# Performance work log

Hardware: AMD Instinct MI355X
Metric: run time of the kernel (lower is better)

The kernel has to match this reference:

```python
import jax, jax.numpy as jnp
import numpy as np

B, W, KD, NC, D, NN, NH, AD, HOPS = 512, 4, 64, 32, 256, 16, 8, 32, 4
DH = D // NH
DFF = 4 * D
P = B * W + B
ROLE_WRITER, ROLE_QUERY = 0, 1


def setup_inputs() -> dict:
    key = jax.random.key(0)
    ks = iter(jax.random.split(key, 40))
    f = lambda shape, s=0.02: jax.random.normal(next(ks), shape, dtype=jnp.float32) * s
    inp = {
        'query_keys': jax.random.normal(next(ks), (B, KD), dtype=jnp.float32),
        'writer_keys': jax.random.normal(next(ks), (B, W, KD), dtype=jnp.float32),
        'key_proj_w': f((KD, D)), 'key_proj_b': jnp.zeros((D,), jnp.float32),
        'class_embed': f((NC, D)), 'role_embed': f((3, D)), 'start_node_embed': f((NN, D)),
        'input_ln_g': jnp.ones((D,), jnp.float32), 'input_ln_b': jnp.zeros((D,), jnp.float32),
        'ln1_g': jnp.ones((NN, D), jnp.float32), 'ln1_b': jnp.zeros((NN, D), jnp.float32),
        'wqkv': f((NN, D, 3 * D)), 'bqkv': jnp.zeros((NN, 3 * D), jnp.float32),
        'wo': f((NN, D, D)), 'bo': jnp.zeros((NN, D), jnp.float32),
        'ln2_g': jnp.ones((NN, D), jnp.float32), 'ln2_b': jnp.zeros((NN, D), jnp.float32),
        'w_fc1': f((NN, D, DFF)), 'b_fc1': jnp.zeros((NN, DFF), jnp.float32),
        'w_fc2': f((NN, DFF, D)), 'b_fc2': jnp.zeros((NN, D), jnp.float32),
        'delta_w': jnp.zeros((D, D), jnp.float32), 'delta_b': jnp.zeros((D,), jnp.float32),
        'dir_w': f((D, D)), 'dir_b': jnp.zeros((D,), jnp.float32),
        'mag_w': f((D, 1)), 'mag_b': jnp.full((1,), 2.5, jnp.float32),
        'out_w': f((D, NC)), 'out_b': jnp.zeros((NC,), jnp.float32),
        'address_table': jax.random.normal(next(ks), (NN, AD), dtype=jnp.float32),
        'query_start_nodes': jax.random.randint(next(ks), (B,), 0, NN),
        'writer_labels': jax.random.randint(next(ks), (B, W), 0, NC),
        'writer_start_nodes': jax.random.randint(next(ks), (B, W), 0, NN),
    }
    return inp


def _ln(x):
    m = jnp.mean(x, -1, keepdims=True)
    v = jnp.var(x, -1, keepdims=True)
    return (x - m) * jax.lax.rsqrt(v + 1e-5)


def _forward(query_keys, writer_keys, key_proj_w, key_proj_b, class_embed, role_embed,
             start_node_embed, input_ln_g, input_ln_b, ln1_g, ln1_b, wqkv, bqkv, wo, bo,
             ln2_g, ln2_b, w_fc1, b_fc1, w_fc2, b_fc2, delta_w, delta_b, dir_w, dir_b,
             mag_w, mag_b, out_w, out_b, address_table,
             query_start_nodes, writer_labels, writer_start_nodes):
    # ---- encode writers (encode_writers) ----
    fk = writer_keys.reshape(-1, KD)          # [B*W, KD]
    fl = writer_labels.reshape(-1)            # [B*W]
    fs = writer_start_nodes.reshape(-1)       # [B*W]
    learned_w = fk @ key_proj_w + key_proj_b + class_embed[fl] + start_node_embed[fs] + role_embed[ROLE_WRITER]
    sw = jnp.zeros_like(learned_w).at[:, :KD].set(fk)
    sw = sw.at[:, KD:KD + NC].set(jax.nn.one_hot(fl, NC, dtype=learned_w.dtype))
    enc_w = _ln(learned_w) * input_ln_g + input_ln_b + sw
    # ---- encode queries (encode_queries) ----
    learned_q = query_keys @ key_proj_w + key_proj_b + start_node_embed[query_start_nodes] + role_embed[ROLE_QUERY]
    sq = jnp.zeros_like(learned_q).at[:, :KD].set(query_keys)
    enc_q = _ln(learned_q) * input_ln_g + input_ln_b + sq

    h = jnp.concatenate([enc_w, enc_q], axis=0)          # [P, D]
    node = jnp.concatenate([fs, query_start_nodes], 0)   # [P] current compute node per packet

    inv_sqrt_dh = 1.0 / np.sqrt(DH).astype(np.float32)
    for _ in range(HOPS):
        oh = jax.nn.one_hot(node, NN, dtype=h.dtype)      # [P, NN] dispatch weights

        def pnl(x, Wn, bn):
            # per-node linear: gather-compute-scatter via MoE-style dense dispatch
            xe = jnp.einsum('pn,pd->npd', oh, x)          # [NN, P, din]
            ye = jnp.einsum('npd,ndf->npf', xe, Wn)       # [NN, P, dout]
            return jnp.einsum('npf,pn->pf', ye, oh) + oh @ bn

        # ComputeNodeCell: pre-LN attention among packets at the same node
        x = _ln(h) * (oh @ ln1_g) + oh @ ln1_b
        qkv = pnl(x, wqkv, bqkv)                          # [P, 3D]
        q, k, v = jnp.split(qkv, 3, axis=-1)
        q = q.reshape(P, NH, DH); k = k.reshape(P, NH, DH); v = v.reshape(P, NH, DH)
        scores = jnp.einsum('phd,qhd->hpq', q, k) * inv_sqrt_dh   # [NH, P, P]
        same = node[:, None] == node[None, :]
        scores = jnp.where(same[None], scores, -1e9)
        attn = jax.nn.softmax(scores, axis=-1)
        ao = jnp.einsum('hpq,qhd->phd', attn, v).reshape(P, D)
        h = h + pnl(ao, wo, bo)
        # MLP block
        x2 = _ln(h) * (oh @ ln2_g) + oh @ ln2_b
        h = h + pnl(jax.nn.gelu(pnl(x2, w_fc1, b_fc1)), w_fc2, b_fc2)
        # routing heads: pick next node from address table, apply gated delta
        direction = h @ dir_w + dir_b
        node = jnp.argmax(direction[:, :AD] @ address_table.T, axis=-1)
        h = h + (h @ delta_w + delta_b) * jax.nn.sigmoid(h @ mag_w + mag_b)

    return h @ out_w + out_b                              # [P, NC] per-packet logits


def reference(query_keys, writer_keys, key_proj_w, key_proj_b, class_embed, role_embed,
              start_node_embed, input_ln_g, input_ln_b, ln1_g, ln1_b, wqkv, bqkv, wo, bo,
              ln2_g, ln2_b, w_fc1, b_fc1, w_fc2, b_fc2, delta_w, delta_b, dir_w, dir_b,
              mag_w, mag_b, out_w, out_b, address_table,
              query_start_nodes, writer_labels, writer_start_nodes):
    return _forward(query_keys, writer_keys, key_proj_w, key_proj_b, class_embed, role_embed,
                    start_node_embed, input_ln_g, input_ln_b, ln1_g, ln1_b, wqkv, bqkv, wo, bo,
                    ln2_g, ln2_b, w_fc1, b_fc1, w_fc2, b_fc2, delta_w, delta_b, dir_w, dir_b,
                    mag_w, mag_b, out_w, out_b, address_table,
                    query_start_nodes, writer_labels, writer_start_nodes)
```

## Files before the change

kernel.cpp:

```cpp
#include <hip/hip_runtime.h>
#include <math.h>

#define B_    512
#define W_    4
#define KD_   64
#define NC_   32
#define D_    256
#define NN_   16
#define NH_   8
#define AD_   32
#define HOPS_ 4
#define DH_   32
#define DFF_  1024
#define P_    2560
#define BW_   2048
#define MAXT_  56
#define MAXT2_ 176
#define PS_   (P_ + 16)

#define INV_SQRT_DH 0.17677669529663687f

typedef __attribute__((ext_vector_type(8))) short short8v;
typedef __attribute__((ext_vector_type(4))) float f32x4;

__device__ __forceinline__ unsigned short bf16_rne(float f) {
  unsigned u = __float_as_uint(f);
  unsigned r = (u + 0x7fffu + ((u >> 16) & 1u)) >> 16;
  return (unsigned short)r;
}
__device__ __forceinline__ void split2(float v, unsigned short& h, unsigned short& l) {
  unsigned short hb = bf16_rne(v);
  float hf = __uint_as_float(((unsigned)hb) << 16);
  h = hb;
  l = bf16_rne(v - hf);
}

__device__ __forceinline__ float block_sum256(float v, float* red) {
#pragma unroll
  for (int off = 32; off > 0; off >>= 1) v += __shfl_xor(v, off, 64);
  int wid = threadIdx.x >> 6;
  if ((threadIdx.x & 63) == 0) red[wid] = v;
  __syncthreads();
  float s = red[0] + red[1] + red[2] + red[3];
  __syncthreads();
  return s;
}

__device__ __forceinline__ float gelu_tanh(float v) {
  float u = 0.7978845608028654f * (v + 0.044715f * v * v * v);
  return 0.5f * v * (1.0f + tanhf(u));
}

__global__ __launch_bounds__(256) void padzero_kernel(unsigned short* __restrict__ xh,
                                                      unsigned short* __restrict__ xl,
                                                      unsigned short* __restrict__ ffh,
                                                      unsigned short* __restrict__ ffl) {
  int t = threadIdx.x;
  for (int i = t; i < 16 * D_; i += 256) {
    xh[(size_t)P_ * D_ + i] = 0;
    xl[(size_t)P_ * D_ + i] = 0;
  }
  for (int i = t; i < 16 * DFF_; i += 256) {
    ffh[(size_t)P_ * DFF_ + i] = 0;
    ffl[(size_t)P_ * DFF_ + i] = 0;
  }
}

__global__ __launch_bounds__(256) void encode_kernel(
    const float* __restrict__ query_keys, const float* __restrict__ writer_keys,
    const float* __restrict__ kpw, const float* __restrict__ kpb,
    const float* __restrict__ ce, const float* __restrict__ re,
    const float* __restrict__ sne, const float* __restrict__ ilg,
    const float* __restrict__ ilb, const int* __restrict__ qsn,
    const int* __restrict__ wl, const int* __restrict__ wsn,
    float* __restrict__ h, int* __restrict__ node) {
  int p = blockIdx.x, t = threadIdx.x;
  __shared__ float fk[KD_];
  __shared__ float red[4];
  const float* key;
  int lab = -1, sn, role;
  if (p < BW_) { key = writer_keys + (size_t)p * KD_; lab = wl[p]; sn = wsn[p]; role = 0; }
  else { int b = p - BW_; key = query_keys + (size_t)b * KD_; sn = qsn[b]; role = 1; }
  if (t < KD_) fk[t] = key[t];
  __syncthreads();

  float acc = kpb[t] + sne[sn * D_ + t] + re[role * D_ + t];
  if (lab >= 0) acc += ce[lab * D_ + t];
#pragma unroll 8
  for (int i = 0; i < KD_; i++) acc += fk[i] * kpw[i * D_ + t];

  float mean = block_sum256(acc, red) * (1.0f / D_);
  float d = acc - mean;
  float var = block_sum256(d * d, red) * (1.0f / D_);
  float xn = d * (1.0f / sqrtf(var + 1e-5f));

  float sw = 0.0f;
  if (t < KD_) sw = fk[t];
  else if (lab >= 0 && t < KD_ + NC_) sw = (t - KD_ == lab) ? 1.0f : 0.0f;

  h[(size_t)p * D_ + t] = xn * ilg[t] + ilb[t] + sw;
  if (t == 0) node[p] = sn;
}

__global__ __launch_bounds__(256) void sort_kernel(const int* __restrict__ node,
                                                   int* __restrict__ order,
                                                   int* __restrict__ invord,
                                                   int* __restrict__ offs,
                                                   int* __restrict__ cnts,
                                                   int* __restrict__ tnode64,
                                                   int* __restrict__ tstart64,
                                                   int* __restrict__ tend64,
                                                   int* __restrict__ ntiles64,
                                                   int* __restrict__ tnode16,
                                                   int* __restrict__ tstart16,
                                                   int* __restrict__ tend16,
                                                   int* __restrict__ ntiles16) {
  __shared__ int c[NN_], o[NN_], cur[NN_];
  int t = threadIdx.x;
  if (t < NN_) c[t] = 0;
  __syncthreads();
  for (int p = t; p < P_; p += 256) atomicAdd(&c[node[p]], 1);
  __syncthreads();
  if (t == 0) {
    int s = 0;
    for (int n = 0; n < NN_; n++) { o[n] = s; cur[n] = s; s += c[n]; }
    int i64 = 0, i16 = 0;
    for (int n = 0; n < NN_; n++) {
      int e = o[n] + c[n];
      for (int m0 = o[n]; m0 < e; m0 += 64) {
        tnode64[i64] = n; tstart64[i64] = m0; tend64[i64] = e; i64++;
      }
      for (int m0 = o[n]; m0 < e; m0 += 16) {
        tnode16[i16] = n; tstart16[i16] = m0; tend16[i16] = e; i16++;
      }
    }
    ntiles64[0] = i64;
    ntiles16[0] = i16;
  }
  __syncthreads();
  if (t < NN_) { cnts[t] = c[t]; offs[t] = o[t]; }
  for (int p = t; p < P_; p += 256) {
    int r = atomicAdd(&cur[node[p]], 1);
    order[r] = p;
    invord[p] = r;
  }
}

__global__ __launch_bounds__(256) void ln_affine(const float* __restrict__ h,
                                                 const float* __restrict__ g,
                                                 const float* __restrict__ b,
                                                 const int* __restrict__ node,
                                                 const int* __restrict__ order,
                                                 unsigned short* __restrict__ xh,
                                                 unsigned short* __restrict__ xl) {
  int sp = blockIdx.x * 4 + (threadIdx.x >> 6);
  int lane = threadIdx.x & 63;
  int p = order[sp];
  int n = node[p];
  float4 v = *(const float4*)&h[(size_t)p * D_ + lane * 4];
  float s = v.x + v.y + v.z + v.w;
#pragma unroll
  for (int off = 32; off > 0; off >>= 1) s += __shfl_xor(s, off, 64);
  float mean = s * (1.0f / D_);
  float4 d = make_float4(v.x - mean, v.y - mean, v.z - mean, v.w - mean);
  float vr = d.x * d.x + d.y * d.y + d.z * d.z + d.w * d.w;
#pragma unroll
  for (int off = 32; off > 0; off >>= 1) vr += __shfl_xor(vr, off, 64);
  float inv = 1.0f / sqrtf(vr * (1.0f / D_) + 1e-5f);
  float4 gg = *(const float4*)&g[n * D_ + lane * 4];
  float4 bb = *(const float4*)&b[n * D_ + lane * 4];
  float o[4];
  o[0] = d.x * inv * gg.x + bb.x;
  o[1] = d.y * inv * gg.y + bb.y;
  o[2] = d.z * inv * gg.z + bb.z;
  o[3] = d.w * inv * gg.w + bb.w;
  ushort4 oh, ol;
  split2(o[0], oh.x, ol.x);
  split2(o[1], oh.y, ol.y);
  split2(o[2], oh.z, ol.z);
  split2(o[3], oh.w, ol.w);
  *(ushort4*)&xh[(size_t)sp * D_ + lane * 4] = oh;
  *(ushort4*)&xl[(size_t)sp * D_ + lane * 4] = ol;
}

template <int K, int C>
__global__ __launch_bounds__(256) void wprep(const float* __restrict__ W,
                                             unsigned short* __restrict__ th,
                                             unsigned short* __restrict__ tl) {
  __shared__ float ld[32][33];
  int n = blockIdx.z;
  int k0 = blockIdx.x * 32, c0 = blockIdx.y * 32;
  int tx = threadIdx.x & 31, ty = threadIdx.x >> 5;
  const float* Wn = W + (size_t)n * K * C;
#pragma unroll
  for (int i = 0; i < 32; i += 8)
    ld[i + ty][tx] = Wn[(size_t)(k0 + i + ty) * C + c0 + tx];
  __syncthreads();
#pragma unroll
  for (int i = 0; i < 32; i += 8) {
    float v = ld[tx][i + ty];
    unsigned short hh, ll;
    split2(v, hh, ll);
    size_t off = ((size_t)n * C + c0 + i + ty) * K + k0 + tx;
    th[off] = hh;
    tl[off] = ll;
  }
}

template <int DIN, int DOUT, int ACT, int RESID, int SPLITOUT>
__global__ __launch_bounds__(256) void gmfma(
    const unsigned short* __restrict__ xh, const unsigned short* __restrict__ xl,
    const unsigned short* __restrict__ wth, const unsigned short* __restrict__ wtl,
    const float* __restrict__ bias, float* __restrict__ outf,
    unsigned short* __restrict__ outh, unsigned short* __restrict__ outl,
    const int* __restrict__ order, const int* __restrict__ tnode,
    const int* __restrict__ tstart, const int* __restrict__ tend,
    const int* __restrict__ ntiles) {
  constexpr int NCH = DIN / 64;
  __shared__ unsigned short ws[2][2][64][64];

  int gx = gridDim.x;
  int bid = blockIdx.x;
  int ti = (bid & 7) * (gx >> 3) + (bid >> 3);
  if (ti >= ntiles[0]) return;
  int n = tnode[ti];
  int s0 = tstart[ti];
  int rows = tend[ti] - s0;
  if (rows <= 0) return;
  if (rows > 16) rows = 16;

  int tid = threadIdx.x;
  int wv = tid >> 6;
  int lane = tid & 63;
  int r16 = lane & 15;
  int kg = lane >> 4;
  int jb = blockIdx.y * 64;

  const unsigned short* wsrc[4];
  int sj[4], c0j[4];
#pragma unroll
  for (int jj = 0; jj < 4; jj++) {
    int j = wv * 4 + jj;
    int s = j >> 3;
    int c0 = (j & 7) * 8;
    int c = c0 + (lane >> 3);
    int e = (lane & 7) ^ (c & 7);
    wsrc[jj] = ((e & 4) ? wtl : wth) +
               ((size_t)(n * DOUT + jb + c)) * DIN + s * 32 + (e & 3) * 8;
    sj[jj] = s;
    c0j[jj] = c0;
  }
  auto stage = [&](int buf, int kbase) {
#pragma unroll
    for (int jj = 0; jj < 4; jj++) {
      __builtin_amdgcn_global_load_lds(
          (const __attribute__((address_space(1))) unsigned int*)(wsrc[jj] + kbase),
          (__attribute__((address_space(3))) unsigned int*)&ws[buf][sj[jj]][c0j[jj]][0],
          16, 0, 0);
    }
  };

  const unsigned short* pah = xh + (size_t)(s0 + r16) * DIN + kg * 8;
  const unsigned short* pal = xl + (size_t)(s0 + r16) * DIN + kg * 8;

  short8v ah[2], al[2], nh[2], nl[2];
  auto afetch = [&](int kbase, short8v (&h_)[2], short8v (&l_)[2]) {
#pragma unroll
    for (int s = 0; s < 2; s++) {
      h_[s] = *(const short8v*)(pah + kbase + s * 32);
      l_[s] = *(const short8v*)(pal + kbase + s * 32);
    }
  };

  f32x4 acc0 = {0.f, 0.f, 0.f, 0.f};
  f32x4 acc1 = acc0, acc2 = acc0;
  int lcol = wv * 16 + r16;
  int ghi_ = (kg ^ (r16 & 7)) * 8;
  int glo_ = ((4 + kg) ^ (r16 & 7)) * 8;

  stage(0, 0);
  afetch(0, ah, al);
  __syncthreads();

  for (int ch = 0; ch < NCH; ch++) {
    int cur = ch & 1;
    if (ch + 1 < NCH) {
      stage(cur ^ 1, (ch + 1) * 64);
      afetch((ch + 1) * 64, nh, nl);
    }
#pragma unroll
    for (int s = 0; s < 2; s++) {
      short8v bh = *(const short8v*)&ws[cur][s][lcol][ghi_];
      short8v bl = *(const short8v*)&ws[cur][s][lcol][glo_];
      acc0 = __builtin_amdgcn_mfma_f32_16x16x32_bf16(ah[s], bh, acc0, 0, 0, 0);
      acc1 = __builtin_amdgcn_mfma_f32_16x16x32_bf16(ah[s], bl, acc1, 0, 0, 0);
      acc2 = __builtin_amdgcn_mfma_f32_16x16x32_bf16(al[s], bh, acc2, 0, 0, 0);
    }
    __syncthreads();
    if (ch + 1 < NCH) {
#pragma unroll
      for (int s = 0; s < 2; s++) { ah[s] = nh[s]; al[s] = nl[s]; }
    }
  }

  int jcol = jb + wv * 16;
  float bv = bias[(size_t)n * DOUT + jcol + r16];
#pragma unroll
  for (int rg = 0; rg < 4; rg++) {
    int r = kg * 4 + rg;
    if (r >= rows) continue;
    float v = acc0[rg] + acc1[rg] + acc2[rg] + bv;
    if (ACT) v = gelu_tanh(v);
    if (SPLITOUT) {
      size_t off = (size_t)(s0 + r) * DOUT + jcol + r16;
      unsigned short hh, ll;
      split2(v, hh, ll);
      outh[off] = hh;
      outl[off] = ll;
    } else if (RESID) {
      int pp = order[s0 + r];
      float* op = outf + (size_t)pp * DOUT + jcol + r16;
      *op += v;
    } else {
      outf[(size_t)(s0 + r) * DOUT + jcol + r16] = v;
    }
  }
}

template <int DIN, int DOUT, int JT, int ACT, int RESID, int PER_NODE, int KSPLIT, int XMODE>
__global__ __launch_bounds__(256) void glin(const float* __restrict__ x,
                                            const float* __restrict__ W,
                                            const float* __restrict__ bias,
                                            float* __restrict__ out,
                                            float* __restrict__ pbuf,
                                            const float* __restrict__ xaux,
                                            const int* __restrict__ order,
                                            const int* __restrict__ invord,
                                            const int* __restrict__ tnode,
                                            const int* __restrict__ tstart,
                                            const int* __restrict__ tend,
                                            const int* __restrict__ ntiles) {
  constexpr int KC = 32, STX = 68;
  constexpr int CPT = JT / 16;
  constexpr int HALF = 64;
  constexpr int KLEN = DIN / KSPLIT;
  constexpr int NCH = KLEN / KC;
  constexpr int LPR = JT / 4;
  constexpr int RPI = 64 / LPR;

  int ti = blockIdx.x;
  int n, s0, s1;
  if (PER_NODE) {
    if (ti >= ntiles[0]) return;
    n = tnode[ti]; s0 = tstart[ti]; s1 = tend[ti];
  } else {
    n = 0; s0 = ti * 64; s1 = P_;
  }
  int jbase = blockIdx.y * JT;
  int kz = (KSPLIT > 1) ? blockIdx.z : 0;
  int k0 = kz * KLEN;
  int rows = s1 - s0; if (rows > 64) rows = 64;

  __shared__ float xs[2][KC][STX];
  __shared__ float ws[2][KC][JT];

  int tid = threadIdx.x;
  const float* Wn = W + (size_t)n * DIN * DOUT + jbase;

  int xrow = tid >> 2, xq = tid & 3;
  bool xvalid = xrow < rows;
  const float* xptr = x + (size_t)(s0 + (xvalid ? xrow : 0)) * DIN + k0 + xq * 4;
  const float* aptr = nullptr;
  if (XMODE == 1) {
    int pr = xvalid ? invord[s0 + xrow] : 0;
    aptr = xaux + (size_t)pr * DIN + k0 + xq * 4;
  }

  float4 xr0, xr1;
  auto xfetch = [&](int kc) {
    if (xvalid) {
      xr0 = *(const float4*)(xptr + kc);
      xr1 = *(const float4*)(xptr + kc + 16);
      if (XMODE == 1) {
        float4 p0 = *(const float4*)(aptr + kc);
        float4 p1 = *(const float4*)(aptr + kc + 16);
        xr0.x += p0.x; xr0.y += p0.y; xr0.z += p0.z; xr0.w += p0.w;
        xr1.x += p1.x; xr1.y += p1.y; xr1.z += p1.z; xr1.w += p1.w;
      }
    } else {
      xr0 = make_float4(0.f, 0.f, 0.f, 0.f);
      xr1 = make_float4(0.f, 0.f, 0.f, 0.f);
    }
  };
  auto xstage = [&](int buf) {
    xs[buf][xq * 4 + 0][xrow] = xr0.x;
    xs[buf][xq * 4 + 1][xrow] = xr0.y;
    xs[buf][xq * 4 + 2][xrow] = xr0.z;
    xs[buf][xq * 4 + 3][xrow] = xr0.w;
    xs[buf][xq * 4 + 16][xrow] = xr1.x;
    xs[buf][xq * 4 + 17][xrow] = xr1.y;
    xs[buf][xq * 4 + 18][xrow] = xr1.z;
    xs[buf][xq * 4 + 19][xrow] = xr1.w;
  };
  int wvw = tid >> 6, lane = tid & 63;
  int wlr = lane / LPR;
  int wlc = (lane % LPR) * 4;
  auto wfetch = [&](int buf, int kc) {
#pragma unroll
    for (int i = 0; i < 8 / RPI; i++) {
      int kr = wvw * 8 + i * RPI;
      const float* g = &Wn[(size_t)(k0 + kc + kr + wlr) * DOUT + wlc];
      __builtin_amdgcn_global_load_lds(
          (const __attribute__((address_space(1))) unsigned int*)g,
          (__attribute__((address_space(3))) unsigned int*)&ws[buf][kr][0],
          16, 0, 0);
    }
  };

  wfetch(0, 0);
  xfetch(0);
  xstage(0);
  __syncthreads();

  int r4 = (tid >> 4) * 4;
  int jc4 = (tid & 15) * 4;
  float acc[4][CPT];
#pragma unroll
  for (int r = 0; r < 4; r++)
#pragma unroll
    for (int cc = 0; cc < CPT; cc++) acc[r][cc] = 0.f;

  for (int c = 0; c < NCH; c++) {
    int cur = c & 1;
    if (c + 1 < NCH) {
      wfetch(cur ^ 1, (c + 1) * KC);
      xfetch((c + 1) * KC);
    }
#pragma unroll 8
    for (int k = 0; k < KC; k++) {
      float4 a = *(const float4*)&xs[cur][k][r4];
      float av[4] = {a.x, a.y, a.z, a.w};
      float bv[CPT];
      float4 b0 = *(const float4*)&ws[cur][k][jc4];
      bv[0] = b0.x; bv[1] = b0.y; bv[2] = b0.z; bv[3] = b0.w;
      if (CPT == 8) {
        float4 b1 = *(const float4*)&ws[cur][k][jc4 + HALF];
        bv[4] = b1.x; bv[5] = b1.y; bv[6] = b1.z; bv[7] = b1.w;
      }
#pragma unroll
      for (int r = 0; r < 4; r++)
#pragma unroll
        for (int cc = 0; cc < CPT; cc++) acc[r][cc] += av[r] * bv[cc];
    }
    if (c + 1 < NCH) xstage(cur ^ 1);
    __syncthreads();
  }

  bool main_part = (KSPLIT == 1) || (kz == 0);
  float bbv[CPT];
#pragma unroll
  for (int cc = 0; cc < 4; cc++) bbv[cc] = bias[n * DOUT + jbase + jc4 + cc];
  if (CPT == 8) {
#pragma unroll
    for (int cc = 0; cc < 4; cc++) bbv[4 + cc] = bias[n * DOUT + jbase + jc4 + HALF + cc];
  }

#pragma unroll
  for (int r = 0; r < 4; r++) {
    int lr = r4 + r;
    if (lr >= rows) continue;
    float v[CPT];
    if (main_part) {
#pragma unroll
      for (int cc = 0; cc < CPT; cc++) {
        v[cc] = acc[r][cc] + bbv[cc];
        if (ACT == 1) v[cc] = gelu_tanh(v[cc]);
      }
      if (RESID) {
        int pp = PER_NODE ? order[s0 + lr] : (s0 + lr);
        float* op = &out[(size_t)pp * DOUT + jbase + jc4];
        {
          float4 old = *(const float4*)op;
          *(float4*)op = make_float4(v[0] + old.x, v[1] + old.y, v[2] + old.z, v[3] + old.w);
        }
        if (CPT == 8) {
          float4 old = *(const float4*)(op + HALF);
          *(float4*)(op + HALF) =
              make_float4(v[4] + old.x, v[5] + old.y, v[6] + old.z, v[7] + old.w);
        }
      } else {
        float* op = &out[(size_t)(s0 + lr) * DOUT + jbase + jc4];
        *(float4*)op = make_float4(v[0], v[1], v[2], v[3]);
        if (CPT == 8)
          *(float4*)(op + HALF) = make_float4(v[4], v[5], v[6], v[7]);
      }
    } else {
      float* op = &pbuf[(size_t)(s0 + lr) * DOUT + jbase + jc4];
      *(float4*)op = make_float4(acc[r][0], acc[r][1], acc[r][2], acc[r][3]);
      if (CPT == 8)
        *(float4*)(op + HALF) = make_float4(acc[r][4], acc[r][5], acc[r][6], acc[r][7]);
    }
  }
}

#define ATS 36
__global__ __launch_bounds__(256) void attn_kernel(const float* __restrict__ qkv,
                                                   const int* __restrict__ node,
                                                   const int* __restrict__ order,
                                                   const int* __restrict__ offs,
                                                   const int* __restrict__ cnts,
                                                   float* __restrict__ ao) {
  __shared__ float qs[32 * ATS];
  __shared__ float kts[32 * ATS];
  __shared__ float vs[32 * ATS];
  __shared__ float ps[32 * ATS];
  __shared__ int glo[32], ghi[32];

  int t = threadIdx.x;
  int r = t >> 3;
  int j4 = (t & 7) * 4;
  int r0 = blockIdx.x * 32;
  int hd = blockIdx.y;

  if (t < 32) {
    int n = node[order[r0 + t]];
    glo[t] = offs[n];
    ghi[t] = offs[n] + cnts[n];
  }
  __syncthreads();

  {
    const float* qp = &qkv[(size_t)(r0 + r) * 768 + hd * 32 + j4];
    float4 q4 = *(const float4*)qp;
    q4.x *= INV_SQRT_DH; q4.y *= INV_SQRT_DH; q4.z *= INV_SQRT_DH; q4.w *= INV_SQRT_DH;
    *(float4*)&qs[r * ATS + j4] = q4;
  }

  int lo = glo[0];
  int hi = ghi[31];
  int myglo = glo[r], myghi = ghi[r];

  float4 o4 = {0.f, 0.f, 0.f, 0.f};
  float mrow = -1e30f, lrow = 0.f;

  for (int kt = lo; kt < hi; kt += 32) {
    int sj = kt + r;
    float4 k4 = {0.f, 0.f, 0.f, 0.f}, v4 = {0.f, 0.f, 0.f, 0.f};
    if (sj < hi) {
      const float* kp = &qkv[(size_t)sj * 768 + 256 + hd * 32 + j4];
      k4 = *(const float4*)kp;
      v4 = *(const float4*)(kp + 256);
    }
    __syncthreads();
    kts[(j4 + 0) * ATS + r] = k4.x;
    kts[(j4 + 1) * ATS + r] = k4.y;
    kts[(j4 + 2) * ATS + r] = k4.z;
    kts[(j4 + 3) * ATS + r] = k4.w;
    *(float4*)&vs[r * ATS + j4] = v4;
    __syncthreads();

    float s0 = 0.f, s1 = 0.f, s2 = 0.f, s3 = 0.f;
#pragma unroll 8
    for (int d = 0; d < 32; d++) {
      float qv = qs[r * ATS + d];
      float4 kv = *(const float4*)&kts[d * ATS + j4];
      s0 += qv * kv.x; s1 += qv * kv.y; s2 += qv * kv.z; s3 += qv * kv.w;
    }
    int c0 = kt + j4;
    if (c0 + 0 < myglo || c0 + 0 >= myghi) s0 = -1e30f;
    if (c0 + 1 < myglo || c0 + 1 >= myghi) s1 = -1e30f;
    if (c0 + 2 < myglo || c0 + 2 >= myghi) s2 = -1e30f;
    if (c0 + 3 < myglo || c0 + 3 >= myghi) s3 = -1e30f;

    float mx = fmaxf(fmaxf(s0, s1), fmaxf(s2, s3));
#pragma unroll
    for (int off = 4; off > 0; off >>= 1) mx = fmaxf(mx, __shfl_xor(mx, off, 8));
    float mnew = fmaxf(mrow, mx);
    float alpha = __expf(mrow - mnew);
    float p0 = __expf(s0 - mnew), p1 = __expf(s1 - mnew);
    float p2 = __expf(s2 - mnew), p3 = __expf(s3 - mnew);
    float ls = p0 + p1 + p2 + p3;
#pragma unroll
    for (int off = 4; off > 0; off >>= 1) ls += __shfl_xor(ls, off, 8);
    lrow = lrow * alpha + ls;
    mrow = mnew;
    o4.x *= alpha; o4.y *= alpha; o4.z *= alpha; o4.w *= alpha;

    *(float4*)&ps[r * ATS + j4] = make_float4(p0, p1, p2, p3);
#pragma unroll 8
    for (int j = 0; j < 32; j++) {
      float pj = ps[r * ATS + j];
      float4 vv = *(const float4*)&vs[j * ATS + j4];
      o4.x += pj * vv.x; o4.y += pj * vv.y; o4.z += pj * vv.z; o4.w += pj * vv.w;
    }
  }

  float inv = 1.f / lrow;
  o4.x *= inv; o4.y *= inv; o4.z *= inv; o4.w *= inv;
  *(float4*)&ao[(size_t)(r0 + r) * D_ + hd * 32 + j4] = o4;
}

__global__ __launch_bounds__(256) void route_kernel(float* __restrict__ h,
                                                    const float* __restrict__ dir_w,
                                                    const float* __restrict__ dir_b,
                                                    const float* __restrict__ at,
                                                    const float* __restrict__ mag_w,
                                                    const float* __restrict__ mag_b,
                                                    const float* __restrict__ delta,
                                                    int* __restrict__ node) {
  int p = blockIdx.x, t = threadIdx.x;
  __shared__ float hs[D_];
  __shared__ float dpart[8][AD_];
  __shared__ float dirs[AD_];
  __shared__ float scs[NN_];
  __shared__ float red[4];
  float hv = h[(size_t)p * D_ + t];
  hs[t] = hv;
  __syncthreads();

  int j = t & 31, seg = t >> 5;
  float part = 0.0f;
#pragma unroll 8
  for (int i = 0; i < 32; i++) {
    int ii = seg * 32 + i;
    part += hs[ii] * dir_w[ii * D_ + j];
  }
  dpart[seg][j] = part;
  __syncthreads();
  if (t < AD_) {
    float s = dir_b[t];
#pragma unroll
    for (int g = 0; g < 8; g++) s += dpart[g][t];
    dirs[t] = s;
  }
  __syncthreads();
  if (t < NN_) {
    float s = 0.0f;
#pragma unroll
    for (int a = 0; a < AD_; a++) s += dirs[a] * at[t * AD_ + a];
    scs[t] = s;
  }
  __syncthreads();
  if (t == 0) {
    float best = scs[0];
    int arg = 0;
    for (int nn = 1; nn < NN_; nn++)
      if (scs[nn] > best) { best = scs[nn]; arg = nn; }
    node[p] = arg;
  }
  float mag = block_sum256(hv * mag_w[t], red) + mag_b[0];
  float sig = 1.0f / (1.0f + __expf(-mag));
  h[(size_t)p * D_ + t] = hv + delta[(size_t)p * D_ + t] * sig;
}

__global__ __launch_bounds__(256) void out_kernel(const float* __restrict__ h,
                                                  const float* __restrict__ ow,
                                                  const float* __restrict__ ob,
                                                  float* __restrict__ out) {
  int p = blockIdx.x, t = threadIdx.x;
  __shared__ float hs[D_];
  __shared__ float part[8][NC_];
  hs[t] = h[(size_t)p * D_ + t];
  __syncthreads();
  int j = t & 31, seg = t >> 5;
  float s = 0.0f;
#pragma unroll 8
  for (int i = 0; i < 32; i++) {
    int ii = seg * 32 + i;
    s += hs[ii] * ow[ii * NC_ + j];
  }
  part[seg][j] = s;
  __syncthreads();
  if (t < NC_) {
    float r = ob[t];
#pragma unroll
    for (int g = 0; g < 8; g++) r += part[g][t];
    out[(size_t)p * NC_ + t] = r;
  }
}

extern "C" void kernel_launch(void* const* d_in, const int* in_sizes, int n_in,
                              void* d_out, int out_size, void* d_ws, size_t ws_size,
                              hipStream_t stream) {
  (void)in_sizes; (void)n_in; (void)out_size; (void)ws_size;
  const float* query_keys       = (const float*)d_in[0];
  const float* writer_keys      = (const float*)d_in[1];
  const float* key_proj_w       = (const float*)d_in[2];
  const float* key_proj_b       = (const float*)d_in[3];
  const float* class_embed      = (const float*)d_in[4];
  const float* role_embed       = (const float*)d_in[5];
  const float* start_node_embed = (const float*)d_in[6];
  const float* input_ln_g       = (const float*)d_in[7];
  const float* input_ln_b       = (const float*)d_in[8];
  const float* ln1_g            = (const float*)d_in[9];
  const float* ln1_b            = (const float*)d_in[10];
  const float* wqkv             = (const float*)d_in[11];
  const float* bqkv             = (const float*)d_in[12];
  const float* wo               = (const float*)d_in[13];
  const float* bo               = (const float*)d_in[14];
  const float* ln2_g            = (const float*)d_in[15];
  const float* ln2_b            = (const float*)d_in[16];
  const float* w_fc1            = (const float*)d_in[17];
  const float* b_fc1            = (const float*)d_in[18];
  const float* w_fc2            = (const float*)d_in[19];
  const float* b_fc2            = (const float*)d_in[20];
  const float* delta_w          = (const float*)d_in[21];
  const float* delta_b          = (const float*)d_in[22];
  const float* dir_w            = (const float*)d_in[23];
  const float* dir_b            = (const float*)d_in[24];
  const float* mag_w            = (const float*)d_in[25];
  const float* mag_b            = (const float*)d_in[26];
  const float* out_w            = (const float*)d_in[27];
  const float* out_b            = (const float*)d_in[28];
  const float* address_table    = (const float*)d_in[29];
  const int* query_start_nodes  = (const int*)d_in[30];
  const int* writer_labels      = (const int*)d_in[31];
  const int* writer_start_nodes = (const int*)d_in[32];

  uintptr_t basep = (uintptr_t)d_ws;
  auto carve = [&](size_t bytes) {
    basep = (basep + 255) & ~(uintptr_t)255;
    void* r = (void*)basep;
    basep += bytes;
    return r;
  };
  float* h    = (float*)carve((size_t)P_ * D_ * 4);
  float* x    = (float*)carve((size_t)P_ * D_ * 4);
  float* buf1 = (float*)carve((size_t)P_ * 768 * 4);
  unsigned short* xh  = (unsigned short*)carve((size_t)PS_ * D_ * 2);
  unsigned short* xl  = (unsigned short*)carve((size_t)PS_ * D_ * 2);
  unsigned short* ffh = (unsigned short*)carve((size_t)PS_ * DFF_ * 2);
  unsigned short* ffl = (unsigned short*)carve((size_t)PS_ * DFF_ * 2);
  unsigned short* wtqh = (unsigned short*)carve((size_t)NN_ * 768 * 256 * 2);
  unsigned short* wtql = (unsigned short*)carve((size_t)NN_ * 768 * 256 * 2);
  unsigned short* wt1h = (unsigned short*)carve((size_t)NN_ * 1024 * 256 * 2);
  unsigned short* wt1l = (unsigned short*)carve((size_t)NN_ * 1024 * 256 * 2);
  unsigned short* wt2h = (unsigned short*)carve((size_t)NN_ * 256 * 1024 * 2);
  unsigned short* wt2l = (unsigned short*)carve((size_t)NN_ * 256 * 1024 * 2);
  int* node   = (int*)carve(P_ * 4);
  int* order  = (int*)carve(P_ * 4);
  int* invord = (int*)carve(P_ * 4);
  int* offs   = (int*)carve(NN_ * 4);
  int* cnts   = (int*)carve(NN_ * 4);
  int* tnode64  = (int*)carve(MAXT_ * 4);
  int* tstart64 = (int*)carve(MAXT_ * 4);
  int* tend64   = (int*)carve(MAXT_ * 4);
  int* ntiles64 = (int*)carve(4);
  int* tnode16  = (int*)carve(MAXT2_ * 4);
  int* tstart16 = (int*)carve(MAXT2_ * 4);
  int* tend16   = (int*)carve(MAXT2_ * 4);
  int* ntiles16 = (int*)carve(4);

  padzero_kernel<<<1, 256, 0, stream>>>(xh, xl, ffh, ffl);
  wprep<256, 768><<<dim3(8, 24, NN_), 256, 0, stream>>>(wqkv, wtqh, wtql);
  wprep<256, 1024><<<dim3(8, 32, NN_), 256, 0, stream>>>(w_fc1, wt1h, wt1l);
  wprep<1024, 256><<<dim3(32, 8, NN_), 256, 0, stream>>>(w_fc2, wt2h, wt2l);

  encode_kernel<<<P_, 256, 0, stream>>>(query_keys, writer_keys, key_proj_w, key_proj_b,
                                        class_embed, role_embed, start_node_embed,
                                        input_ln_g, input_ln_b, query_start_nodes,
                                        writer_labels, writer_start_nodes, h, node);

  for (int hop = 0; hop < HOPS_; ++hop) {
    sort_kernel<<<1, 256, 0, stream>>>(node, order, invord, offs, cnts,
                                       tnode64, tstart64, tend64, ntiles64,
                                       tnode16, tstart16, tend16, ntiles16);
    ln_affine<<<P_ / 4, 256, 0, stream>>>(h, ln1_g, ln1_b, node, order, xh, xl);
    gmfma<256, 768, 0, 0, 0><<<dim3(MAXT2_, 12), 256, 0, stream>>>(
        xh, xl, wtqh, wtql, bqkv, buf1, nullptr, nullptr, order,
        tnode16, tstart16, tend16, ntiles16);
    attn_kernel<<<dim3(P_ / 32, NH_), 256, 0, stream>>>(buf1, node, order, offs,
                                                        cnts, x );
    glin<256, 256, 64, 0, 1, 1, 1, 0><<<dim3(MAXT_, 4), 256, 0, stream>>>(
        x, wo, bo, h, nullptr, nullptr, order, invord, tnode64, tstart64, tend64,
        ntiles64);
    ln_affine<<<P_ / 4, 256, 0, stream>>>(h, ln2_g, ln2_b, node, order, xh, xl);
    gmfma<256, 1024, 1, 0, 1><<<dim3(MAXT2_, 16), 256, 0, stream>>>(
        xh, xl, wt1h, wt1l, b_fc1, nullptr, ffh, ffl, order,
        tnode16, tstart16, tend16, ntiles16);
    gmfma<1024, 256, 0, 1, 0><<<dim3(MAXT2_, 4), 256, 0, stream>>>(
        ffh, ffl, wt2h, wt2l, b_fc2, h, nullptr, nullptr, order,
        tnode16, tstart16, tend16, ntiles16);
    glin<256, 256, 64, 0, 0, 0, 1, 0><<<dim3(P_ / 64, 4), 256, 0, stream>>>(
        h, delta_w, delta_b, buf1 , nullptr, nullptr, order, invord,
        tnode64, tstart64, tend64, ntiles64);
    route_kernel<<<P_, 256, 0, stream>>>(h, dir_w, dir_b, address_table,
                                         mag_w, mag_b, buf1, node);
  }

  out_kernel<<<P_, 256, 0, stream>>>(h, out_w, out_b, (float*)d_out);
}
```

Measured before the change: 930.9 us.

## Move output and delta projections onto split-bf16 MFMA GEMM, double-buffer attention K/V

Replaces the fp32 FMA glin kernel for the per-node output projection and the dense delta projection with the split-bf16 MFMA gmfma kernel. Attention now writes its output as hi/lo bf16 pairs, and the fc2 residual epilogue also emits a bf16 split of h, so the delta GEMM can read MFMA-ready inputs directly. The attention kernel also double-buffers K/V tiles in shared memory so the next tile's loads overlap the current tile's compute. The cost is extra preprocessing of wo and delta_w into split form and extra stores of the split h.

After: 876.3 us, median of 2. 1.06x faster.

```diff
diff --git a/kernel.cpp b/kernel.cpp
--- a/kernel.cpp
+++ b/kernel.cpp
@@ -14,7 +14,6 @@
 #define DFF_  1024
 #define P_    2560
 #define BW_   2048
-#define MAXT_  56
 #define MAXT2_ 176
 #define PS_   (P_ + 16)
 
@@ -104,13 +103,8 @@
 
 __global__ __launch_bounds__(256) void sort_kernel(const int* __restrict__ node,
                                                    int* __restrict__ order,
-                                                   int* __restrict__ invord,
                                                    int* __restrict__ offs,
                                                    int* __restrict__ cnts,
-                                                   int* __restrict__ tnode64,
-                                                   int* __restrict__ tstart64,
-                                                   int* __restrict__ tend64,
-                                                   int* __restrict__ ntiles64,
                                                    int* __restrict__ tnode16,
                                                    int* __restrict__ tstart16,
                                                    int* __restrict__ tend16,
@@ -124,17 +118,13 @@
   if (t == 0) {
     int s = 0;
     for (int n = 0; n < NN_; n++) { o[n] = s; cur[n] = s; s += c[n]; }
-    int i64 = 0, i16 = 0;
+    int i16 = 0;
     for (int n = 0; n < NN_; n++) {
       int e = o[n] + c[n];
-      for (int m0 = o[n]; m0 < e; m0 += 64) {
-        tnode64[i64] = n; tstart64[i64] = m0; tend64[i64] = e; i64++;
-      }
       for (int m0 = o[n]; m0 < e; m0 += 16) {
         tnode16[i16] = n; tstart16[i16] = m0; tend16[i16] = e; i16++;
       }
     }
-    ntiles64[0] = i64;
     ntiles16[0] = i16;
   }
   __syncthreads();
@@ -142,7 +132,6 @@
   for (int p = t; p < P_; p += 256) {
     int r = atomicAdd(&cur[node[p]], 1);
     order[r] = p;
-    invord[p] = r;
   }
 }
 
@@ -207,12 +196,13 @@
   }
 }
 
-template <int DIN, int DOUT, int ACT, int RESID, int SPLITOUT>
+template <int DIN, int DOUT, int ACT, int RESID, int SPLITOUT, int DENSE, int HSPLIT>
 __global__ __launch_bounds__(256) void gmfma(
     const unsigned short* __restrict__ xh, const unsigned short* __restrict__ xl,
     const unsigned short* __restrict__ wth, const unsigned short* __restrict__ wtl,
     const float* __restrict__ bias, float* __restrict__ outf,
     unsigned short* __restrict__ outh, unsigned short* __restrict__ outl,
+    unsigned short* __restrict__ houth, unsigned short* __restrict__ houtl,
     const int* __restrict__ order, const int* __restrict__ tnode,
     const int* __restrict__ tstart, const int* __restrict__ tend,
     const int* __restrict__ ntiles) {
@@ -222,12 +212,19 @@
   int gx = gridDim.x;
   int bid = blockIdx.x;
   int ti = (bid & 7) * (gx >> 3) + (bid >> 3);
-  if (ti >= ntiles[0]) return;
-  int n = tnode[ti];
-  int s0 = tstart[ti];
-  int rows = tend[ti] - s0;
-  if (rows <= 0) return;
-  if (rows > 16) rows = 16;
+  int n, s0, rows;
+  if (DENSE) {
+    n = 0;
+    s0 = ti * 16;
+    rows = 16;
+  } else {
+    if (ti >= ntiles[0]) return;
+    n = tnode[ti];
+    s0 = tstart[ti];
+    rows = tend[ti] - s0;
+    if (rows <= 0) return;
+    if (rows > 16) rows = 16;
+  }
 
   int tid = threadIdx.x;
   int wv = tid >> 6;
@@ -318,187 +315,18 @@
       outh[off] = hh;
       outl[off] = ll;
     } else if (RESID) {
-      int pp = order[s0 + r];
-      float* op = outf + (size_t)pp * DOUT + jcol + r16;
-      *op += v;
+      int pp = DENSE ? (s0 + r) : order[s0 + r];
+      size_t oidx = (size_t)pp * DOUT + jcol + r16;
+      float nv = outf[oidx] + v;
+      outf[oidx] = nv;
+      if (HSPLIT) {
+        unsigned short hh, ll;
+        split2(nv, hh, ll);
+        houth[oidx] = hh;
+        houtl[oidx] = ll;
+      }
     } else {
       outf[(size_t)(s0 + r) * DOUT + jcol + r16] = v;
-    }
-  }
-}
-
-template <int DIN, int DOUT, int JT, int ACT, int RESID, int PER_NODE, int KSPLIT, int XMODE>
-__global__ __launch_bounds__(256) void glin(const float* __restrict__ x,
-                                            const float* __restrict__ W,
-                                            const float* __restrict__ bias,
-                                            float* __restrict__ out,
-                                            float* __restrict__ pbuf,
-                                            const float* __restrict__ xaux,
-                                            const int* __restrict__ order,
-                                            const int* __restrict__ invord,
-                                            const int* __restrict__ tnode,
-                                            const int* __restrict__ tstart,
-                                            const int* __restrict__ tend,
-                                            const int* __restrict__ ntiles) {
-  constexpr int KC = 32, STX = 68;
-  constexpr int CPT = JT / 16;
-  constexpr int HALF = 64;
-  constexpr int KLEN = DIN / KSPLIT;
-  constexpr int NCH = KLEN / KC;
-  constexpr int LPR = JT / 4;
-  constexpr int RPI = 64 / LPR;
-
-  int ti = blockIdx.x;
-  int n, s0, s1;
-  if (PER_NODE) {
-    if (ti >= ntiles[0]) return;
-    n = tnode[ti]; s0 = tstart[ti]; s1 = tend[ti];
-  } else {
-    n = 0; s0 = ti * 64; s1 = P_;
-  }
-  int jbase = blockIdx.y * JT;
-  int kz = (KSPLIT > 1) ? blockIdx.z : 0;
-  int k0 = kz * KLEN;
-  int rows = s1 - s0; if (rows > 64) rows = 64;
-
-  __shared__ float xs[2][KC][STX];
-  __shared__ float ws[2][KC][JT];
-
-  int tid = threadIdx.x;
-  const float* Wn = W + (size_t)n * DIN * DOUT + jbase;
-
-  int xrow = tid >> 2, xq = tid & 3;
-  bool xvalid = xrow < rows;
-  const float* xptr = x + (size_t)(s0 + (xvalid ? xrow : 0)) * DIN + k0 + xq * 4;
-  const float* aptr = nullptr;
-  if (XMODE == 1) {
-    int pr = xvalid ? invord[s0 + xrow] : 0;
-    aptr = xaux + (size_t)pr * DIN + k0 + xq * 4;
-  }
-
-  float4 xr0, xr1;
-  auto xfetch = [&](int kc) {
-    if (xvalid) {
-      xr0 = *(const float4*)(xptr + kc);
-      xr1 = *(const float4*)(xptr + kc + 16);
-      if (XMODE == 1) {
-        float4 p0 = *(const float4*)(aptr + kc);
-        float4 p1 = *(const float4*)(aptr + kc + 16);
-        xr0.x += p0.x; xr0.y += p0.y; xr0.z += p0.z; xr0.w += p0.w;
-        xr1.x += p1.x; xr1.y += p1.y; xr1.z += p1.z; xr1.w += p1.w;
-      }
-    } else {
-      xr0 = make_float4(0.f, 0.f, 0.f, 0.f);
-      xr1 = make_float4(0.f, 0.f, 0.f, 0.f);
-    }
-  };
-  auto xstage = [&](int buf) {
-    xs[buf][xq * 4 + 0][xrow] = xr0.x;
-    xs[buf][xq * 4 + 1][xrow] = xr0.y;
-    xs[buf][xq * 4 + 2][xrow] = xr0.z;
-    xs[buf][xq * 4 + 3][xrow] = xr0.w;
-    xs[buf][xq * 4 + 16][xrow] = xr1.x;
-    xs[buf][xq * 4 + 17][xrow] = xr1.y;
-    xs[buf][xq * 4 + 18][xrow] = xr1.z;
-    xs[buf][xq * 4 + 19][xrow] = xr1.w;
-  };
-  int wvw = tid >> 6, lane = tid & 63;
-  int wlr = lane / LPR;
-  int wlc = (lane % LPR) * 4;
-  auto wfetch = [&](int buf, int kc) {
-#pragma unroll
-    for (int i = 0; i < 8 / RPI; i++) {
-      int kr = wvw * 8 + i * RPI;
-      const float* g = &Wn[(size_t)(k0 + kc + kr + wlr) * DOUT + wlc];
-      __builtin_amdgcn_global_load_lds(
-          (const __attribute__((address_space(1))) unsigned int*)g,
-          (__attribute__((address_space(3))) unsigned int*)&ws[buf][kr][0],
-          16, 0, 0);
-    }
-  };
-
-  wfetch(0, 0);
-  xfetch(0);
-  xstage(0);
-  __syncthreads();
-
-  int r4 = (tid >> 4) * 4;
-  int jc4 = (tid & 15) * 4;
-  float acc[4][CPT];
-#pragma unroll
-  for (int r = 0; r < 4; r++)
-#pragma unroll
-    for (int cc = 0; cc < CPT; cc++) acc[r][cc] = 0.f;
-
-  for (int c = 0; c < NCH; c++) {
-    int cur = c & 1;
-    if (c + 1 < NCH) {
-      wfetch(cur ^ 1, (c + 1) * KC);
-      xfetch((c + 1) * KC);
-    }
-#pragma unroll 8
-    for (int k = 0; k < KC; k++) {
-      float4 a = *(const float4*)&xs[cur][k][r4];
-      float av[4] = {a.x, a.y, a.z, a.w};
-      float bv[CPT];
-      float4 b0 = *(const float4*)&ws[cur][k][jc4];
-      bv[0] = b0.x; bv[1] = b0.y; bv[2] = b0.z; bv[3] = b0.w;
-      if (CPT == 8) {
-        float4 b1 = *(const float4*)&ws[cur][k][jc4 + HALF];
-        bv[4] = b1.x; bv[5] = b1.y; bv[6] = b1.z; bv[7] = b1.w;
-      }
-#pragma unroll
-      for (int r = 0; r < 4; r++)
-#pragma unroll
-        for (int cc = 0; cc < CPT; cc++) acc[r][cc] += av[r] * bv[cc];
-    }
-    if (c + 1 < NCH) xstage(cur ^ 1);
-    __syncthreads();
-  }
-
-  bool main_part = (KSPLIT == 1) || (kz == 0);
-  float bbv[CPT];
-#pragma unroll
-  for (int cc = 0; cc < 4; cc++) bbv[cc] = bias[n * DOUT + jbase + jc4 + cc];
-  if (CPT == 8) {
-#pragma unroll
-    for (int cc = 0; cc < 4; cc++) bbv[4 + cc] = bias[n * DOUT + jbase + jc4 + HALF + cc];
-  }
-
-#pragma unroll
-  for (int r = 0; r < 4; r++) {
-    int lr = r4 + r;
-    if (lr >= rows) continue;
-    float v[CPT];
-    if (main_part) {
-#pragma unroll
-      for (int cc = 0; cc < CPT; cc++) {
-        v[cc] = acc[r][cc] + bbv[cc];
-        if (ACT == 1) v[cc] = gelu_tanh(v[cc]);
-      }
-      if (RESID) {
-        int pp = PER_NODE ? order[s0 + lr] : (s0 + lr);
-        float* op = &out[(size_t)pp * DOUT + jbase + jc4];
-        {
-          float4 old = *(const float4*)op;
-          *(float4*)op = make_float4(v[0] + old.x, v[1] + old.y, v[2] + old.z, v[3] + old.w);
-        }
-        if (CPT == 8) {
-          float4 old = *(const float4*)(op + HALF);
-          *(float4*)(op + HALF) =
-              make_float4(v[4] + old.x, v[5] + old.y, v[6] + old.z, v[7] + old.w);
-        }
-      } else {
-        float* op = &out[(size_t)(s0 + lr) * DOUT + jbase + jc4];
-        *(float4*)op = make_float4(v[0], v[1], v[2], v[3]);
-        if (CPT == 8)
-          *(float4*)(op + HALF) = make_float4(v[4], v[5], v[6], v[7]);
-      }
-    } else {
-      float* op = &pbuf[(size_t)(s0 + lr) * DOUT + jbase + jc4];
-      *(float4*)op = make_float4(acc[r][0], acc[r][1], acc[r][2], acc[r][3]);
-      if (CPT == 8)
-        *(float4*)(op + HALF) = make_float4(acc[r][4], acc[r][5], acc[r][6], acc[r][7]);
     }
   }
 }
@@ -509,10 +337,11 @@
                                                    const int* __restrict__ order,
                                                    const int* __restrict__ offs,
                                                    const int* __restrict__ cnts,
-                                                   float* __restrict__ ao) {
+                                                   unsigned short* __restrict__ aoh,
+                                                   unsigned short* __restrict__ aol) {
   __shared__ float qs[32 * ATS];
-  __shared__ float kts[32 * ATS];
-  __shared__ float vs[32 * ATS];
+  __shared__ float kts[2][32 * ATS];
+  __shared__ float vs[2][32 * ATS];
   __shared__ float ps[32 * ATS];
   __shared__ int glo[32], ghi[32];
 
@@ -539,31 +368,47 @@
   int lo = glo[0];
   int hi = ghi[31];
   int myglo = glo[r], myghi = ghi[r];
-
-  float4 o4 = {0.f, 0.f, 0.f, 0.f};
-  float mrow = -1e30f, lrow = 0.f;
-
-  for (int kt = lo; kt < hi; kt += 32) {
-    int sj = kt + r;
+  int nt = (hi - lo + 31) >> 5;
+
+  {
+    int sj = lo + r;
     float4 k4 = {0.f, 0.f, 0.f, 0.f}, v4 = {0.f, 0.f, 0.f, 0.f};
     if (sj < hi) {
       const float* kp = &qkv[(size_t)sj * 768 + 256 + hd * 32 + j4];
       k4 = *(const float4*)kp;
       v4 = *(const float4*)(kp + 256);
     }
-    __syncthreads();
-    kts[(j4 + 0) * ATS + r] = k4.x;
-    kts[(j4 + 1) * ATS + r] = k4.y;
-    kts[(j4 + 2) * ATS + r] = k4.z;
-    kts[(j4 + 3) * ATS + r] = k4.w;
-    *(float4*)&vs[r * ATS + j4] = v4;
-    __syncthreads();
+    kts[0][(j4 + 0) * ATS + r] = k4.x;
+    kts[0][(j4 + 1) * ATS + r] = k4.y;
+    kts[0][(j4 + 2) * ATS + r] = k4.z;
+    kts[0][(j4 + 3) * ATS + r] = k4.w;
+    *(float4*)&vs[0][r * ATS + j4] = v4;
+  }
+  __syncthreads();
+
+  float4 o4 = {0.f, 0.f, 0.f, 0.f};
+  float mrow = -1e30f, lrow = 0.f;
+
+  for (int it = 0; it < nt; ++it) {
+    int cb = it & 1;
+    int kt = lo + it * 32;
+    bool more = (it + 1 < nt);
+
+    float4 kn = {0.f, 0.f, 0.f, 0.f}, vn = {0.f, 0.f, 0.f, 0.f};
+    if (more) {
+      int sj = kt + 32 + r;
+      if (sj < hi) {
+        const float* kp = &qkv[(size_t)sj * 768 + 256 + hd * 32 + j4];
+        kn = *(const float4*)kp;
+        vn = *(const float4*)(kp + 256);
+      }
+    }
 
     float s0 = 0.f, s1 = 0.f, s2 = 0.f, s3 = 0.f;
 #pragma unroll 8
     for (int d = 0; d < 32; d++) {
       float qv = qs[r * ATS + d];
-      float4 kv = *(const float4*)&kts[d * ATS + j4];
+      float4 kv = *(const float4*)&kts[cb][d * ATS + j4];
       s0 += qv * kv.x; s1 += qv * kv.y; s2 += qv * kv.z; s3 += qv * kv.w;
     }
     int c0 = kt + j4;
@@ -590,14 +435,30 @@
 #pragma unroll 8
     for (int j = 0; j < 32; j++) {
       float pj = ps[r * ATS + j];
-      float4 vv = *(const float4*)&vs[j * ATS + j4];
+      float4 vv = *(const float4*)&vs[cb][j * ATS + j4];
       o4.x += pj * vv.x; o4.y += pj * vv.y; o4.z += pj * vv.z; o4.w += pj * vv.w;
+    }
+
+    if (more) {
+      kts[cb ^ 1][(j4 + 0) * ATS + r] = kn.x;
+      kts[cb ^ 1][(j4 + 1) * ATS + r] = kn.y;
+      kts[cb ^ 1][(j4 + 2) * ATS + r] = kn.z;
+      kts[cb ^ 1][(j4 + 3) * ATS + r] = kn.w;
+      *(float4*)&vs[cb ^ 1][r * ATS + j4] = vn;
+      __syncthreads();
     }
   }
 
   float inv = 1.f / lrow;
   o4.x *= inv; o4.y *= inv; o4.z *= inv; o4.w *= inv;
-  *(float4*)&ao[(size_t)(r0 + r) * D_ + hd * 32 + j4] = o4;
+  ushort4 oh4, ol4;
+  split2(o4.x, oh4.x, ol4.x);
+  split2(o4.y, oh4.y, ol4.y);
+  split2(o4.z, oh4.z, ol4.z);
+  split2(o4.w, oh4.w, ol4.w);
+  size_t off = (size_t)(r0 + r) * D_ + hd * 32 + j4;
+  *(ushort4*)&aoh[off] = oh4;
+  *(ushort4*)&aol[off] = ol4;
 }
 
 __global__ __launch_bounds__(256) void route_kernel(float* __restrict__ h,
@@ -725,27 +586,27 @@
     return r;
   };
   float* h    = (float*)carve((size_t)P_ * D_ * 4);
-  float* x    = (float*)carve((size_t)P_ * D_ * 4);
   float* buf1 = (float*)carve((size_t)P_ * 768 * 4);
   unsigned short* xh  = (unsigned short*)carve((size_t)PS_ * D_ * 2);
   unsigned short* xl  = (unsigned short*)carve((size_t)PS_ * D_ * 2);
   unsigned short* ffh = (unsigned short*)carve((size_t)PS_ * DFF_ * 2);
   unsigned short* ffl = (unsigned short*)carve((size_t)PS_ * DFF_ * 2);
+  unsigned short* hh  = (unsigned short*)carve((size_t)P_ * D_ * 2);
+  unsigned short* hl  = (unsigned short*)carve((size_t)P_ * D_ * 2);
   unsigned short* wtqh = (unsigned short*)carve((size_t)NN_ * 768 * 256 * 2);
   unsigned short* wtql = (unsigned short*)carve((size_t)NN_ * 768 * 256 * 2);
   unsigned short* wt1h = (unsigned short*)carve((size_t)NN_ * 1024 * 256 * 2);
   unsigned short* wt1l = (unsigned short*)carve((size_t)NN_ * 1024 * 256 * 2);
   unsigned short* wt2h = (unsigned short*)carve((size_t)NN_ * 256 * 1024 * 2);
   unsigned short* wt2l = (unsigned short*)carve((size_t)NN_ * 256 * 1024 * 2);
+  unsigned short* wtoh = (unsigned short*)carve((size_t)NN_ * 256 * 256 * 2);
+  unsigned short* wtol = (unsigned short*)carve((size_t)NN_ * 256 * 256 * 2);
+  unsigned short* dth  = (unsigned short*)carve((size_t)256 * 256 * 2);
+  unsigned short* dtl  = (unsigned short*)carve((size_t)256 * 256 * 2);
   int* node   = (int*)carve(P_ * 4);
   int* order  = (int*)carve(P_ * 4);
-  int* invord = (int*)carve(P_ * 4);
   int* offs   = (int*)carve(NN_ * 4);
   int* cnts   = (int*)carve(NN_ * 4);
-  int* tnode64  = (int*)carve(MAXT_ * 4);
-  int* tstart64 = (int*)carve(MAXT_ * 4);
-  int* tend64   = (int*)carve(MAXT_ * 4);
-  int* ntiles64 = (int*)carve(4);
   int* tnode16  = (int*)carve(MAXT2_ * 4);
   int* tstart16 = (int*)carve(MAXT2_ * 4);
   int* tend16   = (int*)carve(MAXT2_ * 4);
@@ -755,6 +616,8 @@
   wprep<256, 768><<<dim3(8, 24, NN_), 256, 0, stream>>>(wqkv, wtqh, wtql);
   wprep<256, 1024><<<dim3(8, 32, NN_), 256, 0, stream>>>(w_fc1, wt1h, wt1l);
   wprep<1024, 256><<<dim3(32, 8, NN_), 256, 0, stream>>>(w_fc2, wt2h, wt2l);
+  wprep<256, 256><<<dim3(8, 8, NN_), 256, 0, stream>>>(wo, wtoh, wtol);
+  wprep<256, 256><<<dim3(8, 8, 1), 256, 0, stream>>>(delta_w, dth, dtl);
 
   encode_kernel<<<P_, 256, 0, stream>>>(query_keys, writer_keys, key_proj_w, key_proj_b,
                                         class_embed, role_embed, start_node_embed,
@@ -762,28 +625,27 @@
                                         writer_labels, writer_start_nodes, h, node);
 
   for (int hop = 0; hop < HOPS_; ++hop) {
-    sort_kernel<<<1, 256, 0, stream>>>(node, order, invord, offs, cnts,
-                                       tnode64, tstart64, tend64, ntiles64,
+    sort_kernel<<<1, 256, 0, stream>>>(node, order, offs, cnts,
                                        tnode16, tstart16, tend16, ntiles16);
     ln_affine<<<P_ / 4, 256, 0, stream>>>(h, ln1_g, ln1_b, node, order, xh, xl);
-    gmfma<256, 768, 0, 0, 0><<<dim3(MAXT2_, 12), 256, 0, stream>>>(
-        xh, xl, wtqh, wtql, bqkv, buf1, nullptr, nullptr, order,
-        tnode16, tstart16, tend16, ntiles16);
+    gmfma<256, 768, 0, 0, 0, 0, 0><<<dim3(MAXT2_, 12), 256, 0, stream>>>(
+        xh, xl, wtqh, wtql, bqkv, buf1, nullptr, nullptr, nullptr, nullptr,
+        order, tnode16, tstart16, tend16, ntiles16);
     attn_kernel<<<dim3(P_ / 32, NH_), 256, 0, stream>>>(buf1, node, order, offs,
-                                                        cnts, x );
-    glin<256, 256, 64, 0, 1, 1, 1, 0><<<dim3(MAXT_, 4), 256, 0, stream>>>(
-        x, wo, bo, h, nullptr, nullptr, order, invord, tnode64, tstart64, tend64,
-        ntiles64);
+                                                        cnts, xh, xl);
+    gmfma<256, 256, 0, 1, 0, 0, 0><<<dim3(MAXT2_, 4), 256, 0, stream>>>(
+        xh, xl, wtoh, wtol, bo, h, nullptr, nullptr, nullptr, nullptr,
+        order, tnode16, tstart16, tend16, ntiles16);
     ln_affine<<<P_ / 4, 256, 0, stream>>>(h, ln2_g, ln2_b, node, order, xh, xl);
-    gmfma<256, 1024, 1, 0, 1><<<dim3(MAXT2_, 16), 256, 0, stream>>>(
-        xh, xl, wt1h, wt1l, b_fc1, nullptr, ffh, ffl, order,
-        tnode16, tstart16, tend16, ntiles16);
-    gmfma<1024, 256, 0, 1, 0><<<dim3(MAXT2_, 4), 256, 0, stream>>>(
-        ffh, ffl, wt2h, wt2l, b_fc2, h, nullptr, nullptr, order,
-        tnode16, tstart16, tend16, ntiles16);
-    glin<256, 256, 64, 0, 0, 0, 1, 0><<<dim3(P_ / 64, 4), 256, 0, stream>>>(
-        h, delta_w, delta_b, buf1 , nullptr, nullptr, order, invord,
-        tnode64, tstart64, tend64, ntiles64);
+    gmfma<256, 1024, 1, 0, 1, 0, 0><<<dim3(MAXT2_, 16), 256, 0, stream>>>(
+        xh, xl, wt1h, wt1l, b_fc1, nullptr, ffh, ffl, nullptr, nullptr,
+        order, tnode16, tstart16, tend16, ntiles16);
+    gmfma<1024, 256, 0, 1, 0, 0, 1><<<dim3(MAXT2_, 4), 256, 0, stream>>>(
+        ffh, ffl, wt2h, wt2l, b_fc2, h, nullptr, nullptr, hh, hl,
+        order, tnode16, tstart16, tend16, ntiles16);
+    gmfma<256, 256, 0, 0, 0, 1, 0><<<dim3(P_ / 16, 4), 256, 0, stream>>>(
+        hh, hl, dth, dtl, delta_b, buf1, nullptr, nullptr, nullptr, nullptr,
+        order, tnode16, tstart16, tend16, ntiles16);
     route_kernel<<<P_, 256, 0, stream>>>(h, dir_w, dir_b, address_table,
                                          mag_w, mag_b, buf1, node);
   }
```
